# Kernel tuning notes

Measured on AMD Instinct MI355X. Metric: run time of the kernel, lower is better.

Reference implementation:

```python
import jax, jax.numpy as jnp
import numpy as np

B, S, D, H, T, MAXLEN = 8, 1024, 768, 12, 384, 1024
HD = D // H  # spatial head dim = 64
SCALE = HD ** -0.5


def setup_inputs() -> dict:
    key = jax.random.key(0)
    ks = jax.random.split(key, 16)

    def lin(k, din, dout):
        kw, _ = jax.random.split(k)
        w = jax.random.normal(kw, (din, dout), jnp.float32) / np.sqrt(din).astype(np.float32)
        b = jnp.zeros((dout,), jnp.float32)
        return w, b

    Wqs, bqs = lin(ks[0], D, D)
    Wks, bks = lin(ks[1], D, D)
    Wvs, bvs = lin(ks[2], D, D)
    Wqt, bqt = lin(ks[3], T, D)
    Wkt, bkt = lin(ks[4], T, D)
    Wvt, bvt = lin(ks[5], T, D)
    Er = jax.random.normal(ks[6], (MAXLEN, HD), jnp.float32)
    patches = jax.random.normal(ks[7], (B, S, D), jnp.float32)
    time_emb = jax.random.normal(ks[8], (B, T), jnp.float32)
    return dict(patches=patches, time_emb=time_emb,
                Wqs=Wqs, bqs=bqs, Wks=Wks, bks=bks, Wvs=Wvs, bvs=bvs,
                Wqt=Wqt, bqt=bqt, Wkt=Wkt, bkt=bkt, Wvt=Wvt, bvt=bvt, Er=Er)


def _skew(QEr):
    # QEr: [B, H, S, S] -> pad one zero col on the left, reshape, drop first row.
    b, h, r, c = QEr.shape
    padded = jnp.pad(QEr, ((0, 0), (0, 0), (0, 0), (1, 0)))  # [B,H,r,c+1]
    reshaped = padded.reshape(b, h, c + 1, r)
    return reshaped[:, :, 1:, :]  # [B,H,S,S]


def reference(patches, time_emb, Wqs, bqs, Wks, bks, Wvs, bvs,
              Wqt, bqt, Wkt, bkt, Wvt, bvt, Er):
    b, s, _ = patches.shape

    def heads(x):  # [B,S,D] -> [B,H,S,HD]
        return x.reshape(b, -1, H, HD).transpose(0, 2, 1, 3)

    qs = heads(patches @ Wqs + bqs)
    ks = heads(patches @ Wks + bks)
    vs = heads(patches @ Wvs + bvs)
    qt = heads(time_emb @ Wqt + bqt)  # [B,H,1,HD]
    kt = heads(time_emb @ Wkt + bkt)
    vt = heads(time_emb @ Wvt + bvt)

    q = qs + qt
    k = ks + kt
    v = vs + vt

    Er_slice = Er[MAXLEN - s:, :]                      # [S, HD]
    QEr = jnp.einsum('bhsd,td->bhst', qs, Er_slice)    # [B,H,S,S]
    Srel = _skew(QEr)

    scores = (jnp.einsum('bhqd,bhkd->bhqk', q, k) + Srel) * SCALE
    attn = jax.nn.softmax(scores, axis=-1)
    out = jnp.einsum('bhqk,bhkd->bhqd', attn, v)       # [B,H,S,HD]
    return out.transpose(0, 2, 1, 3).reshape(b, s, H * HD)
```

## Files before the change

### kernel.cpp

```cpp
#include <hip/hip_runtime.h>

typedef __attribute__((ext_vector_type(8))) short short8;
typedef __attribute__((ext_vector_type(4))) float floatx4;

#define CSC 0.1803368801f

__device__ __forceinline__ unsigned short f2b(float f){
  unsigned int u = __builtin_bit_cast(unsigned int, f);
  unsigned int r = (u + 0x7fffu + ((u >> 16) & 1u)) >> 16;
  return (unsigned short)r;
}
__device__ __forceinline__ float b2f(unsigned short h){
  unsigned int u = ((unsigned int)h) << 16;
  return __builtin_bit_cast(float, u);
}
__device__ __forceinline__ floatx4 mfma16(short8 a, short8 b, floatx4 c){
  return __builtin_amdgcn_mfma_f32_16x16x32_bf16(a, b, c, 0, 0, 0);
}
__device__ __forceinline__ void gload_lds16(const unsigned short* g, unsigned short* l){
  __builtin_amdgcn_global_load_lds(
      (const __attribute__((address_space(1))) unsigned int*)g,
      (__attribute__((address_space(3))) unsigned int*)l, 16, 0, 0);
}

__global__ __launch_bounds__(256) void prep_kernel(
    const float* __restrict__ patches, const float* __restrict__ Er,
    const float* __restrict__ temb,
    const float* __restrict__ Wqt, const float* __restrict__ bqt,
    const float* __restrict__ Wkt, const float* __restrict__ bkt,
    const float* __restrict__ Wvt, const float* __restrict__ bvt,
    const float* __restrict__ Wqs, const float* __restrict__ Wks,
    const float* __restrict__ Wvs,
    unsigned short* __restrict__ Pb, unsigned short* __restrict__ Erb,
    float* __restrict__ Tmat, unsigned short* __restrict__ Wb){
  int blk = blockIdx.x, tid = threadIdx.x;
  if (blk < 3104){
    const float* src; unsigned short* dst; int idx;
    if (blk < 3072){ idx = blk*2048 + tid*8; src = patches; dst = Pb; }
    else           { idx = (blk-3072)*2048 + tid*8; src = Er; dst = Erb; }
    float4 f0 = *(const float4*)(src + idx);
    float4 f1 = *(const float4*)(src + idx + 4);
    uint4 pk;
    pk.x = (unsigned)f2b(f0.x) | ((unsigned)f2b(f0.y)<<16);
    pk.y = (unsigned)f2b(f0.z) | ((unsigned)f2b(f0.w)<<16);
    pk.z = (unsigned)f2b(f1.x) | ((unsigned)f2b(f1.y)<<16);
    pk.w = (unsigned)f2b(f1.z) | ((unsigned)f2b(f1.w)<<16);
    *(uint4*)(dst + idx) = pk;
  } else if (blk < 3128){
    int g = (blk-3104)>>3, bb = (blk-3104)&7;
    const float* Wt = (g==0)? Wqt : (g==1)? Wkt : Wvt;
    const float* bt = (g==0)? bqt : (g==1)? bkt : bvt;
    __shared__ float emb[384];
    for (int j=tid;j<384;j+=256) emb[j] = temb[bb*384 + j];
    __syncthreads();
    float acc0 = bt[tid], acc1 = bt[tid+256], acc2 = bt[tid+512];
    #pragma unroll 4
    for (int t=0;t<384;t++){
      float e = emb[t];
      const float* wr = Wt + t*768;
      acc0 += e*wr[tid]; acc1 += e*wr[tid+256]; acc2 += e*wr[tid+512];
    }
    float* dst = Tmat + g*6144 + bb*768;
    float s = (g==0) ? CSC : 1.0f;
    dst[tid] = acc0*s; dst[tid+256] = acc1*s; dst[tid+512] = acc2*s;
  } else {
    int tb = blk - 3128;
    int g = tb / 144, rem = tb % 144;
    int by = rem / 12, bx = rem % 12;
    __shared__ float tile[64][65];
    const float* W = (g==0) ? Wqs : (g==1) ? Wks : Wvs;
    int r0 = by*64, c0 = bx*64;
    int tx = tid & 63, ty = tid >> 6;
    #pragma unroll
    for (int i=0;i<16;i++){
      int r = i*4 + ty;
      tile[r][tx] = W[(r0+r)*768 + c0 + tx];
    }
    __syncthreads();
    unsigned short* dst = Wb + g*589824;
    #pragma unroll
    for (int i=0;i<16;i++){
      int rr = i*4 + ty;
      dst[(c0+rr)*768 + r0 + tx] = f2b(tile[tx][rr]);
    }
  }
}

__global__ __launch_bounds__(256) void qkv_gemm(
    const unsigned short* __restrict__ Pb, const unsigned short* __restrict__ Wb,
    const float* __restrict__ bq, const float* __restrict__ bk,
    const float* __restrict__ bv, const float* __restrict__ Tmat,
    unsigned short* __restrict__ Qs, unsigned short* __restrict__ K,
    unsigned short* __restrict__ V){
  __shared__ unsigned short smem_q[32768];
  int g = blockIdx.z;
  int m0 = blockIdx.x*128, n0 = blockIdx.y*128;
  int tid = threadIdx.x, w = tid>>6, lane = tid&63, quad = lane>>4, l16 = lane&15;
  int wr = w>>1, wc = w&1;
  const unsigned short* Wg = Wb + g*589824;
  const float* bias = (g==0)? bq : (g==1)? bk : bv;
  floatx4 acc[4][4];
  #pragma unroll
  for (int i=0;i<4;i++)
    #pragma unroll
    for (int j=0;j<4;j++) acc[i][j] = (floatx4){0.f,0.f,0.f,0.f};

  int rsub = lane>>3;
  int csw  = (((lane&7) ^ rsub) << 3);
  int sw   = l16 & 7;

  #pragma unroll
  for (int j=0;j<4;j++){
    int chunk = w*4 + j;
    int r = chunk*8 + rsub;
    gload_lds16(&Pb[(m0+r)*768 + csw],        &smem_q[chunk*512]);
    gload_lds16(&Wg[(n0+r)*768 + csw],        &smem_q[8192 + chunk*512]);
  }
  __syncthreads();

  int cur = 0;
  for (int kt=0; kt<12; kt++){
    if (kt < 11){
      int k0n = (kt+1)*64;
      unsigned short* an = smem_q + (cur^1)*16384;
      unsigned short* bn = an + 8192;
      #pragma unroll
      for (int j=0;j<4;j++){
        int chunk = w*4 + j;
        int r = chunk*8 + rsub;
        gload_lds16(&Pb[(m0+r)*768 + k0n + csw], &an[chunk*512]);
        gload_lds16(&Wg[(n0+r)*768 + k0n + csw], &bn[chunk*512]);
      }
    }
    const unsigned short* a_lds = smem_q + cur*16384;
    const unsigned short* b_lds = a_lds + 8192;
    #pragma unroll
    for (int ks=0; ks<2; ks++){
      short8 af[4], bf[4];
      int cc = ((ks*4 + quad) ^ sw) << 3;
      #pragma unroll
      for (int mb=0;mb<4;mb++)
        af[mb] = *(const short8*)&a_lds[(wr*64+mb*16+l16)*64 + cc];
      #pragma unroll
      for (int nb=0;nb<4;nb++)
        bf[nb] = *(const short8*)&b_lds[(wc*64+nb*16+l16)*64 + cc];
      #pragma unroll
      for (int mb=0;mb<4;mb++)
        #pragma unroll
        for (int nb=0;nb<4;nb++)
          acc[mb][nb] = mfma16(af[mb], bf[nb], acc[mb][nb]);
    }
    __syncthreads();
    cur ^= 1;
  }
  if (g < 2){
    #pragma unroll
    for (int mb=0;mb<4;mb++)
    #pragma unroll
    for (int nb=0;nb<4;nb++)
    #pragma unroll
    for (int reg=0;reg<4;reg++){
      int m = m0 + wr*64 + mb*16 + quad*4 + reg;
      int n = n0 + wc*64 + nb*16 + l16;
      int bb = m >> 10, s = m & 1023, h = n >> 6, hd = n & 63;
      float v = acc[mb][nb][reg] + bias[n];
      int base = (bb*12 + h) << 16;
      if (g == 0){
        Qs[base + (s<<6) + hd] = f2b(v * CSC);
      } else {
        float tadd = Tmat[6144 + bb*768 + n];
        K[base + (s<<6) + hd] = f2b(v + tadd);
      }
    }
  } else {
    int bb = m0 >> 10;
    #pragma unroll
    for (int mb=0;mb<4;mb++)
    #pragma unroll
    for (int nb=0;nb<4;nb++)
    #pragma unroll
    for (int reg=0;reg<4;reg++){
      int ml = wr*64 + mb*16 + quad*4 + reg;
      int nl = wc*64 + nb*16 + l16;
      int n = n0 + nl;
      float v = acc[mb][nb][reg] + bias[n] + Tmat[12288 + bb*768 + n];
      smem_q[nl*136 + ml] = f2b(v);
    }
    __syncthreads();
    int s0 = m0 & 1023;
    #pragma unroll
    for (int i=0;i<8;i++){
      int idx = i*256 + tid;
      int r = idx >> 4, c8 = (idx & 15) << 3;
      int n = n0 + r, h = n >> 6, hd = n & 63;
      int base = (bb*12 + h) << 16;
      *(uint4*)&V[base + (hd<<10) + s0 + c8] = *(const uint4*)&smem_q[r*136 + c8];
    }
  }
}

__global__ __launch_bounds__(256, 3) void attn_kernel(
    const unsigned short* __restrict__ Qsp, const unsigned short* __restrict__ Kp,
    const unsigned short* __restrict__ Vtp, const unsigned short* __restrict__ Erb,
    const float* __restrict__ Tq, float* __restrict__ out){
  __shared__ __align__(16) char smem[29696];
  unsigned short* k_lds  = (unsigned short*)smem;
  unsigned short* v_lds  = (unsigned short*)(smem + 9216);
  unsigned short* pw_all = (unsigned short*)(smem + 18432);

  int tid = threadIdx.x, w = tid>>6, lane = tid&63, quad = lane>>4, l16 = lane&15;
  unsigned short* pw = pw_all + w*1408;
  int wg = blockIdx.x;
  int b = wg & 7, slot = wg >> 3;
  int h = slot >> 3, q0 = (slot & 7) << 7;
  int hb = (b*12 + h) << 16;
  const unsigned short* Qsh = Qsp + hb;
  const unsigned short* Kh  = Kp  + hb;
  const unsigned short* Vh  = Vtp + hb;
  const float* tqv = Tq + b*768 + h*64;

  int frow = w*16 + l16;
  short8 qf[2][2], qlo[2][2], qhi[2][2];
  #pragma unroll
  for (int sub=0; sub<2; sub++){
    int qrow = q0 + sub*64 + frow;
    int qrow1 = (qrow < 1023) ? qrow+1 : 1023;
    #pragma unroll
    for (int ks=0; ks<2; ks++){
      int c = ks*32 + quad*8;
      qlo[sub][ks] = *(const short8*)&Qsh[(qrow <<6) + c];
      qhi[sub][ks] = *(const short8*)&Qsh[(qrow1<<6) + c];
      float4 t0 = *(const float4*)&tqv[c];
      float4 t1 = *(const float4*)&tqv[c+4];
      short8 qq;
      qq[0]=(short)f2b(b2f((unsigned short)qlo[sub][ks][0])+t0.x);
      qq[1]=(short)f2b(b2f((unsigned short)qlo[sub][ks][1])+t0.y);
      qq[2]=(short)f2b(b2f((unsigned short)qlo[sub][ks][2])+t0.z);
      qq[3]=(short)f2b(b2f((unsigned short)qlo[sub][ks][3])+t0.w);
      qq[4]=(short)f2b(b2f((unsigned short)qlo[sub][ks][4])+t1.x);
      qq[5]=(short)f2b(b2f((unsigned short)qlo[sub][ks][5])+t1.y);
      qq[6]=(short)f2b(b2f((unsigned short)qlo[sub][ks][6])+t1.z);
      qq[7]=(short)f2b(b2f((unsigned short)qlo[sub][ks][7])+t1.w);
      qf[sub][ks] = qq;
    }
  }

  float lpart[2][4] = {{0.f,0.f,0.f,0.f},{0.f,0.f,0.f,0.f}};
  floatx4 o_acc[2][4];
  #pragma unroll
  for (int sub=0;sub<2;sub++)
    #pragma unroll
    for (int ob=0;ob<4;ob++) o_acc[sub][ob] = (floatx4){0.f,0.f,0.f,0.f};

  int ql = quad*4;
  int ub_lo = 3 - w;

  int sr = tid>>3, scc = (tid&7)<<3;
  uint4 kr0, kr1, vr0, vr1;
  kr0 = *(const uint4*)&Kh[(sr<<6) + scc];
  kr1 = *(const uint4*)&Kh[((sr+32)<<6) + scc];
  vr0 = *(const uint4*)&Vh[(sr<<10) + scc];
  vr1 = *(const uint4*)&Vh[((sr+32)<<10) + scc];

  for (int kt=0; kt<16; kt++){
    int k0 = kt*64;
    __syncthreads();
    *(uint4*)&k_lds[sr*72 + scc]      = kr0;
    *(uint4*)&k_lds[(sr+32)*72 + scc] = kr1;
    *(uint4*)&v_lds[sr*72 + scc]      = vr0;
    *(uint4*)&v_lds[(sr+32)*72 + scc] = vr1;
    __syncthreads();
    int k0n = (kt < 15) ? k0 + 64 : k0;
    kr0 = *(const uint4*)&Kh[((k0n+sr)<<6) + scc];
    kr1 = *(const uint4*)&Kh[((k0n+sr+32)<<6) + scc];
    vr0 = *(const uint4*)&Vh[(sr<<10) + k0n + scc];
    vr1 = *(const uint4*)&Vh[((sr+32)<<10) + k0n + scc];

    floatx4 sc[2][4];
    __builtin_amdgcn_s_setprio(1);
    #pragma unroll
    for (int nb=0;nb<4;nb++){
      sc[0][nb] = (floatx4){0.f,0.f,0.f,0.f};
      sc[1][nb] = (floatx4){0.f,0.f,0.f,0.f};
      #pragma unroll
      for (int ks=0;ks<2;ks++){
        short8 kf = *(const short8*)&k_lds[(nb*16+l16)*72 + ks*32 + quad*8];
        sc[0][nb] = mfma16(qf[0][ks], kf, sc[0][nb]);
        sc[1][nb] = mfma16(qf[1][ks], kf, sc[1][nb]);
      }
    }
    __builtin_amdgcn_s_setprio(0);

    #pragma unroll
    for (int sub=0; sub<2; sub++){
      int diag = k0 - q0 - sub*64;
      bool needL = (diag <= 0), needU = (diag >= 0);
      bool needSel = (diag == 0) || (diag == 64);
      for (int pass=0; pass<2; pass++){
        if ((pass==0 && !needL) || (pass==1 && !needU)) continue;
        int tbase = (pass==0) ? (960 + diag) : (diag - 65);
        const short8* af = (pass==0) ? qlo[sub] : qhi[sub];
        #pragma unroll
        for (int lb=0; lb<5; lb++){
          int ub = ub_lo + lb;
          int t = tbase + ub*16 + l16;
          t = (t < 0) ? 0 : (t > 1023 ? 1023 : t);
          floatx4 pa = (floatx4){0.f,0.f,0.f,0.f};
          #pragma unroll
          for (int ks=0;ks<2;ks++){
            short8 ef = *(const short8*)&Erb[(t<<6) + ks*32 + quad*8];
            pa = mfma16(af[ks], ef, pa);
          }
          #pragma unroll
          for (int reg=0;reg<4;reg++)
            pw[(ql + reg)*88 + lb*16 + l16] = f2b(pa[reg]);
        }
        #pragma unroll
        for (int nb=0;nb<4;nb++)
        #pragma unroll
        for (int reg=0;reg<4;reg++){
          int qlr = ql + reg;
          int ki = nb*16 + l16;
          float bv = b2f(pw[qlr*88 + 15 + ki - qlr]);
          if (needSel){
            int kq = diag + ki - (w*16 + qlr);
            bool sel = (pass==0) ? (kq <= 0) : (kq >= 2);
            bv = sel ? bv : 0.f;
          }
          sc[sub][nb][reg] += bv;
        }
      }
      #pragma unroll
      for (int nb=0;nb<4;nb++)
      #pragma unroll
      for (int reg=0;reg<4;reg++){
        float p = __builtin_amdgcn_exp2f(sc[sub][nb][reg]);
        lpart[sub][reg] += p;
        pw[(ql + reg)*88 + nb*16 + l16] = f2b(p);
      }
      short8 pf[2];
      #pragma unroll
      for (int ks=0;ks<2;ks++)
        pf[ks] = *(const short8*)&pw[l16*88 + ks*32 + quad*8];
      __builtin_amdgcn_s_setprio(1);
      #pragma unroll
      for (int ob=0;ob<4;ob++){
        #pragma unroll
        for (int ks=0;ks<2;ks++){
          short8 vf = *(const short8*)&v_lds[(ob*16+l16)*72 + ks*32 + quad*8];
          o_acc[sub][ob] = mfma16(pf[ks], vf, o_acc[sub][ob]);
        }
      }
      __builtin_amdgcn_s_setprio(0);
    }
  }
  #pragma unroll
  for (int sub=0;sub<2;sub++){
    float rl[4];
    #pragma unroll
    for (int reg=0;reg<4;reg++){
      float l = lpart[sub][reg];
      #pragma unroll
      for (int off=1; off<16; off<<=1) l += __shfl_xor(l, off);
      rl[reg] = __builtin_amdgcn_rcpf(l);
    }
    #pragma unroll
    for (int ob=0;ob<4;ob++)
    #pragma unroll
    for (int reg=0;reg<4;reg++){
      int s = q0 + sub*64 + w*16 + quad*4 + reg;
      out[((b<<10) + s)*768 + (h<<6) + ob*16 + l16] = o_acc[sub][ob][reg] * rl[reg];
    }
  }
}

extern "C" void kernel_launch(void* const* d_in, const int* in_sizes, int n_in,
                              void* d_out, int out_size, void* d_ws, size_t ws_size,
                              hipStream_t stream) {
  const float* patches  = (const float*)d_in[0];
  const float* time_emb = (const float*)d_in[1];
  const float* Wqs = (const float*)d_in[2];  const float* bqs = (const float*)d_in[3];
  const float* Wks = (const float*)d_in[4];  const float* bks = (const float*)d_in[5];
  const float* Wvs = (const float*)d_in[6];  const float* bvs = (const float*)d_in[7];
  const float* Wqt = (const float*)d_in[8];  const float* bqt = (const float*)d_in[9];
  const float* Wkt = (const float*)d_in[10]; const float* bkt = (const float*)d_in[11];
  const float* Wvt = (const float*)d_in[12]; const float* bvt = (const float*)d_in[13];
  const float* Er  = (const float*)d_in[14];

  unsigned short* Qsp  = (unsigned short*)d_ws;
  unsigned short* Kp   = Qsp + 6291456;
  unsigned short* Vp   = Kp  + 6291456;
  unsigned short* Wbp  = Vp  + 6291456;
  unsigned short* Erbp = Wbp + 1769472;
  unsigned short* Pbp  = Erbp + 65536;
  float*          Tmat = (float*)(Pbp + 6291456);

  float* out = (float*)d_out;

  hipLaunchKernelGGL(prep_kernel, dim3(3560), dim3(256), 0, stream,
                     patches, Er, time_emb, Wqt, bqt, Wkt, bkt, Wvt, bvt,
                     Wqs, Wks, Wvs, Pbp, Erbp, Tmat, Wbp);
  hipLaunchKernelGGL(qkv_gemm, dim3(64,6,3), dim3(256), 0, stream,
                     Pbp, Wbp, bqs, bks, bvs, Tmat, Qsp, Kp, Vp);
  hipLaunchKernelGGL(attn_kernel, dim3(768), dim3(256), 0, stream,
                     Qsp, Kp, Vp, Erbp, Tmat, out);
}
```

Measured before the change: 324.6 us.

## Restructure QKV GEMM k-loop into two-stage prefetch with explicit vmcnt waits

Rewrites the QKV GEMM main loop so two K-tiles are always in flight. Explicit s_waitcnt vmcnt counters with raw s_barrier replace the full __syncthreads per iteration, so global-to-LDS loads for tile t+2 overlap compute on tile t. It also adds a launch_bounds occupancy hint of two blocks per CU. The hand-counted vmcnt values and sched barriers are fragile and can create hazards if the compiler reorders or the load counts change; a sync is added before the V epilogue reuses shared memory.

Result: no change. 323.4 us (-0.4%).

```diff
diff --git a/kernel.cpp b/kernel.cpp
--- a/kernel.cpp
+++ b/kernel.cpp
@@ -86,7 +86,7 @@
   }
 }
 
-__global__ __launch_bounds__(256) void qkv_gemm(
+__global__ __launch_bounds__(256, 2) void qkv_gemm(
     const unsigned short* __restrict__ Pb, const unsigned short* __restrict__ Wb,
     const float* __restrict__ bq, const float* __restrict__ bk,
     const float* __restrict__ bv, const float* __restrict__ Tmat,
@@ -109,30 +109,20 @@
   int csw  = (((lane&7) ^ rsub) << 3);
   int sw   = l16 & 7;
 
-  #pragma unroll
-  for (int j=0;j<4;j++){
-    int chunk = w*4 + j;
-    int r = chunk*8 + rsub;
-    gload_lds16(&Pb[(m0+r)*768 + csw],        &smem_q[chunk*512]);
-    gload_lds16(&Wg[(n0+r)*768 + csw],        &smem_q[8192 + chunk*512]);
-  }
-  __syncthreads();
-
-  int cur = 0;
-  for (int kt=0; kt<12; kt++){
-    if (kt < 11){
-      int k0n = (kt+1)*64;
-      unsigned short* an = smem_q + (cur^1)*16384;
-      unsigned short* bn = an + 8192;
-      #pragma unroll
-      for (int j=0;j<4;j++){
-        int chunk = w*4 + j;
-        int r = chunk*8 + rsub;
-        gload_lds16(&Pb[(m0+r)*768 + k0n + csw], &an[chunk*512]);
-        gload_lds16(&Wg[(n0+r)*768 + k0n + csw], &bn[chunk*512]);
-      }
-    }
-    const unsigned short* a_lds = smem_q + cur*16384;
+  auto STAGE = [&](int buf, int kt){
+    int k0 = kt*64;
+    unsigned short* an = smem_q + buf*16384;
+    unsigned short* bn = an + 8192;
+    #pragma unroll
+    for (int j=0;j<4;j++){
+      int chunk = w*4 + j;
+      int r = chunk*8 + rsub;
+      gload_lds16(&Pb[(m0+r)*768 + k0 + csw], &an[chunk*512]);
+      gload_lds16(&Wg[(n0+r)*768 + k0 + csw], &bn[chunk*512]);
+    }
+  };
+  auto COMPUTE = [&](int buf){
+    const unsigned short* a_lds = smem_q + buf*16384;
     const unsigned short* b_lds = a_lds + 8192;
     #pragma unroll
     for (int ks=0; ks<2; ks++){
@@ -150,9 +140,28 @@
         for (int nb=0;nb<4;nb++)
           acc[mb][nb] = mfma16(af[mb], bf[nb], acc[mb][nb]);
     }
-    __syncthreads();
-    cur ^= 1;
-  }
+  };
+
+  STAGE(0, 0);
+  STAGE(1, 1);
+
+  #pragma unroll 2
+  for (int t=0; t<10; t++){
+    asm volatile("s_waitcnt vmcnt(8)" ::: "memory");
+    __builtin_amdgcn_sched_barrier(0);
+    __builtin_amdgcn_s_barrier();
+    COMPUTE(t & 1);
+    asm volatile("s_waitcnt lgkmcnt(0)" ::: "memory");
+    __builtin_amdgcn_sched_barrier(0);
+    __builtin_amdgcn_s_barrier();
+    STAGE(t & 1, t + 2);
+  }
+  asm volatile("s_waitcnt vmcnt(0)" ::: "memory");
+  __builtin_amdgcn_sched_barrier(0);
+  __builtin_amdgcn_s_barrier();
+  COMPUTE(0);
+  COMPUTE(1);
+
   if (g < 2){
     #pragma unroll
     for (int mb=0;mb<4;mb++)
@@ -173,6 +182,7 @@
       }
     }
   } else {
+    __syncthreads();
     int bb = m0 >> 10;
     #pragma unroll
     for (int mb=0;mb<4;mb++)
```

## Split time-projection over K with atomics; widen GEMM N tile, single-buffer LDS

Applied to the files above, without the earlier changes.

The time-embedding projection in the prep kernel is split into six K chunks per (group, batch), which gives 144 blocks instead of 24. Partial sums are combined with atomicAdd into a Tmat buffer that is now zeroed with a memset first, to shorten that serial tail. The QKV GEMM tile grows from 128x128 to 128x192 and drops LDS double buffering so three blocks can fit per CU. The cost is that global-to-LDS loads are no longer overlapped with MFMA work, plus an extra memset launch and float atomics whose order is nondeterministic.

New measurement: 305.9 us, median of 4. 1.06x faster.

```diff
diff --git a/kernel.cpp b/kernel.cpp
--- a/kernel.cpp
+++ b/kernel.cpp
@@ -46,25 +46,29 @@
     pk.z = (unsigned)f2b(f1.x) | ((unsigned)f2b(f1.y)<<16);
     pk.w = (unsigned)f2b(f1.z) | ((unsigned)f2b(f1.w)<<16);
     *(uint4*)(dst + idx) = pk;
-  } else if (blk < 3128){
-    int g = (blk-3104)>>3, bb = (blk-3104)&7;
+  } else if (blk < 3248){
+    int idx = blk - 3104;
+    int g = idx / 48, rem = idx % 48, bb = rem / 6, kc = rem % 6;
     const float* Wt = (g==0)? Wqt : (g==1)? Wkt : Wvt;
     const float* bt = (g==0)? bqt : (g==1)? bkt : bvt;
-    __shared__ float emb[384];
-    for (int j=tid;j<384;j+=256) emb[j] = temb[bb*384 + j];
-    __syncthreads();
-    float acc0 = bt[tid], acc1 = bt[tid+256], acc2 = bt[tid+512];
-    #pragma unroll 4
-    for (int t=0;t<384;t++){
+    __shared__ float emb[64];
+    if (tid < 64) emb[tid] = temb[bb*384 + kc*64 + tid];
+    __syncthreads();
+    float a0 = 0.f, a1 = 0.f, a2 = 0.f;
+    #pragma unroll 8
+    for (int t=0;t<64;t++){
       float e = emb[t];
-      const float* wr = Wt + t*768;
-      acc0 += e*wr[tid]; acc1 += e*wr[tid+256]; acc2 += e*wr[tid+512];
-    }
+      const float* wr = Wt + (kc*64 + t)*768;
+      a0 += e*wr[tid]; a1 += e*wr[tid+256]; a2 += e*wr[tid+512];
+    }
+    if (kc == 0){ a0 += bt[tid]; a1 += bt[tid+256]; a2 += bt[tid+512]; }
+    float s = (g==0) ? CSC : 1.0f;
     float* dst = Tmat + g*6144 + bb*768;
-    float s = (g==0) ? CSC : 1.0f;
-    dst[tid] = acc0*s; dst[tid+256] = acc1*s; dst[tid+512] = acc2*s;
+    atomicAdd(&dst[tid],     a0*s);
+    atomicAdd(&dst[tid+256], a1*s);
+    atomicAdd(&dst[tid+512], a2*s);
   } else {
-    int tb = blk - 3128;
+    int tb = blk - 3248;
     int g = tb / 144, rem = tb % 144;
     int by = rem / 12, bx = rem % 12;
     __shared__ float tile[64][65];
@@ -86,82 +90,73 @@
   }
 }
 
-__global__ __launch_bounds__(256) void qkv_gemm(
+__global__ __launch_bounds__(256, 3) void qkv_gemm(
     const unsigned short* __restrict__ Pb, const unsigned short* __restrict__ Wb,
     const float* __restrict__ bq, const float* __restrict__ bk,
     const float* __restrict__ bv, const float* __restrict__ Tmat,
     unsigned short* __restrict__ Qs, unsigned short* __restrict__ K,
     unsigned short* __restrict__ V){
-  __shared__ unsigned short smem_q[32768];
+  __shared__ unsigned short smem_q[26112];
+  unsigned short* a_lds = smem_q;
+  unsigned short* b_lds = smem_q + 8192;
   int g = blockIdx.z;
-  int m0 = blockIdx.x*128, n0 = blockIdx.y*128;
+  int m0 = blockIdx.x*128, n0 = blockIdx.y*192;
   int tid = threadIdx.x, w = tid>>6, lane = tid&63, quad = lane>>4, l16 = lane&15;
   int wr = w>>1, wc = w&1;
   const unsigned short* Wg = Wb + g*589824;
   const float* bias = (g==0)? bq : (g==1)? bk : bv;
-  floatx4 acc[4][4];
+  floatx4 acc[4][6];
   #pragma unroll
   for (int i=0;i<4;i++)
     #pragma unroll
-    for (int j=0;j<4;j++) acc[i][j] = (floatx4){0.f,0.f,0.f,0.f};
+    for (int j=0;j<6;j++) acc[i][j] = (floatx4){0.f,0.f,0.f,0.f};
 
   int rsub = lane>>3;
   int csw  = (((lane&7) ^ rsub) << 3);
   int sw   = l16 & 7;
 
-  #pragma unroll
-  for (int j=0;j<4;j++){
-    int chunk = w*4 + j;
-    int r = chunk*8 + rsub;
-    gload_lds16(&Pb[(m0+r)*768 + csw],        &smem_q[chunk*512]);
-    gload_lds16(&Wg[(n0+r)*768 + csw],        &smem_q[8192 + chunk*512]);
-  }
-  __syncthreads();
-
-  int cur = 0;
   for (int kt=0; kt<12; kt++){
-    if (kt < 11){
-      int k0n = (kt+1)*64;
-      unsigned short* an = smem_q + (cur^1)*16384;
-      unsigned short* bn = an + 8192;
-      #pragma unroll
-      for (int j=0;j<4;j++){
-        int chunk = w*4 + j;
-        int r = chunk*8 + rsub;
-        gload_lds16(&Pb[(m0+r)*768 + k0n + csw], &an[chunk*512]);
-        gload_lds16(&Wg[(n0+r)*768 + k0n + csw], &bn[chunk*512]);
-      }
-    }
-    const unsigned short* a_lds = smem_q + cur*16384;
-    const unsigned short* b_lds = a_lds + 8192;
+    int k0 = kt*64;
+    __syncthreads();
+    #pragma unroll
+    for (int j=0;j<4;j++){
+      int chunk = w*4 + j;
+      int r = chunk*8 + rsub;
+      gload_lds16(&Pb[(m0+r)*768 + k0 + csw], &a_lds[chunk*512]);
+    }
+    #pragma unroll
+    for (int j=0;j<6;j++){
+      int chunk = w*6 + j;
+      int r = chunk*8 + rsub;
+      gload_lds16(&Wg[(n0+r)*768 + k0 + csw], &b_lds[chunk*512]);
+    }
+    __syncthreads();
     #pragma unroll
     for (int ks=0; ks<2; ks++){
-      short8 af[4], bf[4];
+      short8 af[4], bf[6];
       int cc = ((ks*4 + quad) ^ sw) << 3;
       #pragma unroll
       for (int mb=0;mb<4;mb++)
         af[mb] = *(const short8*)&a_lds[(wr*64+mb*16+l16)*64 + cc];
       #pragma unroll
-      for (int nb=0;nb<4;nb++)
-        bf[nb] = *(const short8*)&b_lds[(wc*64+nb*16+l16)*64 + cc];
+      for (int nb=0;nb<6;nb++)
+        bf[nb] = *(const short8*)&b_lds[(wc*96+nb*16+l16)*64 + cc];
       #pragma unroll
       for (int mb=0;mb<4;mb++)
         #pragma unroll
-        for (int nb=0;nb<4;nb++)
+        for (int nb=0;nb<6;nb++)
           acc[mb][nb] = mfma16(af[mb], bf[nb], acc[mb][nb]);
     }
-    __syncthreads();
-    cur ^= 1;
   }
   if (g < 2){
     #pragma unroll
     for (int mb=0;mb<4;mb++)
     #pragma unroll
-    for (int nb=0;nb<4;nb++)
+    for (int nb=0;nb<6;nb++)
     #pragma unroll
     for (int reg=0;reg<4;reg++){
       int m = m0 + wr*64 + mb*16 + quad*4 + reg;
-      int n = n0 + wc*64 + nb*16 + l16;
+      int n = n0 + wc*96 + nb*16 + l16;
       int bb = m >> 10, s = m & 1023, h = n >> 6, hd = n & 63;
       float v = acc[mb][nb][reg] + bias[n];
       int base = (bb*12 + h) << 16;
@@ -173,15 +168,16 @@
       }
     }
   } else {
+    __syncthreads();
     int bb = m0 >> 10;
     #pragma unroll
     for (int mb=0;mb<4;mb++)
     #pragma unroll
-    for (int nb=0;nb<4;nb++)
+    for (int nb=0;nb<6;nb++)
     #pragma unroll
     for (int reg=0;reg<4;reg++){
       int ml = wr*64 + mb*16 + quad*4 + reg;
-      int nl = wc*64 + nb*16 + l16;
+      int nl = wc*96 + nb*16 + l16;
       int n = n0 + nl;
       float v = acc[mb][nb][reg] + bias[n] + Tmat[12288 + bb*768 + n];
       smem_q[nl*136 + ml] = f2b(v);
@@ -189,7 +185,7 @@
     __syncthreads();
     int s0 = m0 & 1023;
     #pragma unroll
-    for (int i=0;i<8;i++){
+    for (int i=0;i<12;i++){
       int idx = i*256 + tid;
       int r = idx >> 4, c8 = (idx & 15) << 3;
       int n = n0 + r, h = n >> 6, hd = n & 63;
@@ -397,10 +393,11 @@
 
   float* out = (float*)d_out;
 
-  hipLaunchKernelGGL(prep_kernel, dim3(3560), dim3(256), 0, stream,
+  hipMemsetAsync(Tmat, 0, 3*8*768*sizeof(float), stream);
+  hipLaunchKernelGGL(prep_kernel, dim3(3680), dim3(256), 0, stream,
                      patches, Er, time_emb, Wqt, bqt, Wkt, bkt, Wvt, bvt,
                      Wqs, Wks, Wvs, Pbp, Erbp, Tmat, Wbp);
-  hipLaunchKernelGGL(qkv_gemm, dim3(64,6,3), dim3(256), 0, stream,
+  hipLaunchKernelGGL(qkv_gemm, dim3(64,4,3), dim3(256), 0, stream,
                      Pbp, Wbp, bqs, bks, bvs, Tmat, Qsp, Kp, Vp);
   hipLaunchKernelGGL(attn_kernel, dim3(768), dim3(256), 0, stream,
                      Qsp, Kp, Vp, Erbp, Tmat, out);
```
